# Kernel optimization log

Measured on AMD Instinct MI355X. Metric: run time of the kernel, lower is better.

## Reference

```python
import jax, jax.numpy as jnp
import numpy as np

B, T, V = 4096, 32, 256          # batch, decode steps, vocab
E, CE, H, L, NH = 768, 64, 256, 2, 4  # eword_dim, char_emb_dim, hidden, gru layers, heads
HD = H // NH                      # head dim
BOS, PAD = 1, 0


def _gru_cell(x, h, w_ih, w_hh, b_ih, b_hh):
    # PyTorch GRUCell math: gates ordered (r, z, n)
    gi = x @ w_ih.T + b_ih
    gh = h @ w_hh.T + b_hh
    ir, iz, inn = jnp.split(gi, 3, axis=-1)
    hr, hz, hn = jnp.split(gh, 3, axis=-1)
    r = jax.nn.sigmoid(ir + hr)
    z = jax.nn.sigmoid(iz + hz)
    n = jnp.tanh(inn + r * hn)
    return (1.0 - z) * n + z * h


def setup_inputs() -> dict:
    key = jax.random.key(0)
    ks = jax.random.split(key, 24)
    s = 0.02
    p = lambda k, shp: (jax.random.normal(k, shp, jnp.float32) * s)
    return {
        "eword": jax.random.normal(ks[0], (B, E), jnp.float32),
        "target_ids": jax.random.randint(ks[1], (B, T), 0, V),
        # params
        "char_emb": p(ks[2], (V, CE)).at[PAD].set(0.0),
        "eword_proj_w": p(ks[3], (H, E)), "eword_proj_b": p(ks[4], (H,)),
        "gru_w_ih0": p(ks[5], (3 * H, CE + E)), "gru_w_hh0": p(ks[6], (3 * H, H)),
        "gru_b_ih0": p(ks[7], (3 * H,)), "gru_b_hh0": p(ks[8], (3 * H,)),
        "gru_w_ih1": p(ks[9], (3 * H, H)), "gru_w_hh1": p(ks[10], (3 * H, H)),
        "gru_b_ih1": p(ks[11], (3 * H,)), "gru_b_hh1": p(ks[12], (3 * H,)),
        "attn_in_w": p(ks[13], (3 * H, H)), "attn_in_b": p(ks[14], (3 * H,)),
        "attn_out_w": p(ks[15], (H, H)), "attn_out_b": p(ks[16], (H,)),
        "key_w": p(ks[17], (H, E)), "key_b": p(ks[18], (H,)),
        "val_w": p(ks[19], (H, E)), "val_b": p(ks[20], (H,)),
        "proj_w": p(ks[21], (V, H)), "proj_b": p(ks[22], (V,)),
    }


def reference(eword, target_ids, char_emb, eword_proj_w, eword_proj_b,
              gru_w_ih0, gru_w_hh0, gru_b_ih0, gru_b_hh0,
              gru_w_ih1, gru_w_hh1, gru_b_ih1, gru_b_hh1,
              attn_in_w, attn_in_b, attn_out_w, attn_out_b,
              key_w, key_b, val_w, val_b, proj_w, proj_b):
    batch = eword.shape[0]
    # init hidden: tanh(Linear(eword)) broadcast across layers
    h0 = jnp.tanh(eword @ eword_proj_w.T + eword_proj_b)
    # pre-projected key/value (seq len 1), then MHA in-proj for k,v (static)
    wq, wk, wv = jnp.split(attn_in_w, 3, axis=0)
    bq, bk, bv = jnp.split(attn_in_b, 3)
    ek = (eword @ key_w.T + key_b) @ wk.T + bk        # (B, H)
    ev = (eword @ val_w.T + val_b) @ wv.T + bv        # (B, H)
    kh = ek.reshape(batch, NH, HD)                     # (B, NH, HD)
    vh = ev.reshape(batch, NH, HD)
    scale = 1.0 / np.sqrt(HD).astype(np.float32)

    # teacher forcing: input at step t is BOS for t=0, else target_ids[:, t-1]
    in_ids = jnp.concatenate(
        [jnp.full((batch, 1), BOS, target_ids.dtype), target_ids[:, :-1]], axis=1)

    def step(carry, ids):
        h_l0, h_l1 = carry
        ce = char_emb[ids] * (ids != PAD)[:, None].astype(char_emb.dtype)
        x = jnp.concatenate([ce, eword], axis=-1)     # (B, CE+E)
        h_l0 = _gru_cell(x, h_l0, gru_w_ih0, gru_w_hh0, gru_b_ih0, gru_b_hh0)
        h_l1 = _gru_cell(h_l0, h_l1, gru_w_ih1, gru_w_hh1, gru_b_ih1, gru_b_hh1)
        # single-query cross-attention over a length-1 key/value
        q = (h_l1 @ wq.T + bq).reshape(batch, NH, HD)
        score = jnp.sum(q * kh, axis=-1, keepdims=True) * scale  # (B, NH, 1)
        w = jax.nn.softmax(score, axis=-1)            # ones (len-1 softmax)
        attn = (w * vh).reshape(batch, H)
        attn_out = attn @ attn_out_w.T + attn_out_b
        out = h_l1 + attn_out
        logits = out @ proj_w.T + proj_b              # (B, V)
        return (h_l0, h_l1), logits

    _, logits_t = jax.lax.scan(step, (h0, h0), in_ids.T)  # (T, B, V)
    return jnp.transpose(logits_t, (1, 0, 2))              # (B, T, V)
```

## Files before the change

kernel.cpp:

```cpp
#include <hip/hip_runtime.h>


typedef __bf16 bf16;
typedef __attribute__((ext_vector_type(8))) __bf16 bf16x8;
typedef __attribute__((ext_vector_type(4))) __bf16 bf16x4;
typedef __attribute__((ext_vector_type(4))) float fx4;

#define MFMA16(a, b, c) __builtin_amdgcn_mfma_f32_16x16x32_bf16(a, b, c, 0, 0, 0)

__device__ __forceinline__ float sigm(float x) { return 1.0f / (1.0f + expf(-x)); }

__device__ __forceinline__ bf16x8 cvt8(const float* __restrict__ p) {
    float4 u = ((const float4*)p)[0];
    float4 v = ((const float4*)p)[1];
    bf16x8 r;
    r[0] = (bf16)u.x; r[1] = (bf16)u.y; r[2] = (bf16)u.z; r[3] = (bf16)u.w;
    r[4] = (bf16)v.x; r[5] = (bf16)v.y; r[6] = (bf16)v.z; r[7] = (bf16)v.w;
    return r;
}

__device__ __forceinline__ bf16x8 addcvt8(bf16x8 h, const float* __restrict__ p) {
    float4 u = ((const float4*)p)[0];
    float4 v = ((const float4*)p)[1];
    bf16x8 r;
    r[0] = (bf16)((float)h[0] + u.x); r[1] = (bf16)((float)h[1] + u.y);
    r[2] = (bf16)((float)h[2] + u.z); r[3] = (bf16)((float)h[3] + u.w);
    r[4] = (bf16)((float)h[4] + v.x); r[5] = (bf16)((float)h[5] + v.y);
    r[6] = (bf16)((float)h[6] + v.z); r[7] = (bf16)((float)h[7] + v.w);
    return r;
}

__global__ void f2b(const float* __restrict__ s, bf16* __restrict__ d, int n) {
    int i = (blockIdx.x * 256 + threadIdx.x) * 4;
    if (i >= n) return;
    float4 v = *(const float4*)(s + i);
    bf16x4 o;
    o[0] = (bf16)v.x; o[1] = (bf16)v.y; o[2] = (bf16)v.z; o[3] = (bf16)v.w;
    *(bf16x4*)(d + i) = o;
}

__global__ void wpack(const float* __restrict__ src, bf16* __restrict__ dst) {
    int gid = blockIdx.x * 256 + threadIdx.x;
    if (gid >= 768 * 32) return;
    int gc = gid >> 5, piece = gid & 31;
    int g = gc >> 8, rem = gc & 255, w = rem >> 4, l16 = rem & 15;
    int c = piece >> 2, quad = piece & 3;
    bf16x8 v = cvt8(src + (size_t)gc * 256 + piece * 8);
    size_t d = (size_t)w * 12288 + (size_t)(c * 3 + g) * 512 + l16 * 32 + quad * 8;
    *(bf16x8*)(dst + d) = v;
}

__global__ __launch_bounds__(256, 4) void gemm_bt(
    const float* __restrict__ A, int lda,
    const float* __restrict__ W, int ldw,
    const float* __restrict__ bias,
    float* __restrict__ out, int ldo, int act_tanh, int K)
{
    const int tid  = threadIdx.x;
    const int wid  = tid >> 6;
    const int lane = tid & 63;
    const int quad = lane >> 4;
    const int l16  = lane & 15;
    const int m0   = blockIdx.x * 32;
    const int n0   = blockIdx.y * 256 + wid * 64;

    fx4 acc[4][2];
#pragma unroll
    for (int j = 0; j < 4; ++j) {
        acc[j][0] = fx4{0.f, 0.f, 0.f, 0.f};
        acc[j][1] = fx4{0.f, 0.f, 0.f, 0.f};
    }

    const float* a0p = A + (size_t)(m0 + l16) * lda + quad * 8;
    const float* a1p = A + (size_t)(m0 + 16 + l16) * lda + quad * 8;

    for (int k0 = 0; k0 < K; k0 += 32) {
        bf16x8 a0 = cvt8(a0p + k0);
        bf16x8 a1 = cvt8(a1p + k0);
#pragma unroll
        for (int j = 0; j < 4; ++j) {
            bf16x8 b = cvt8(W + (size_t)(n0 + j * 16 + l16) * ldw + k0 + quad * 8);
            acc[j][0] = MFMA16(a0, b, acc[j][0]);
            acc[j][1] = MFMA16(a1, b, acc[j][1]);
        }
    }

#pragma unroll
    for (int j = 0; j < 4; ++j) {
        int n = n0 + j * 16 + l16;
        float bv = bias ? bias[n] : 0.0f;
#pragma unroll
        for (int rt = 0; rt < 2; ++rt)
#pragma unroll
            for (int r = 0; r < 4; ++r) {
                int m = m0 + rt * 16 + quad * 4 + r;
                float v = acc[j][rt][r] + bv;
                if (act_tanh) v = tanhf(v);
                out[(size_t)m * ldo + n] = v;
            }
    }
}

__global__ __launch_bounds__(1024, 4) void decoder_loop(
    const int*   __restrict__ tgt,
    const float* __restrict__ h0i,
    const float* __restrict__ gword,
    const float* __restrict__ cproj,
    const bf16*  __restrict__ w_hh0p, const float* __restrict__ b_hh0,
    const bf16*  __restrict__ w_ih1p, const float* __restrict__ b_ih1,
    const bf16*  __restrict__ w_hh1p, const float* __restrict__ b_hh1,
    bf16* __restrict__ h1all)
{
    __shared__ __align__(16) bf16 hb0[2][16][264];
    __shared__ __align__(16) bf16 hb1[2][16][264];

    const int tid  = threadIdx.x;
    const int wid  = tid >> 6;
    const int lane = tid & 63;
    const int quad = lane >> 4;
    const int l16  = lane & 15;
    const int row0 = blockIdx.x * 16;
    const int col  = wid * 16 + l16;
    const int rw   = quad * 4;

    const bf16* pW0 = w_hh0p + (size_t)wid * 12288 + l16 * 32 + quad * 8;
    const bf16* pW1 = w_ih1p + (size_t)wid * 12288 + l16 * 32 + quad * 8;
    const bf16* pW2 = w_hh1p + (size_t)wid * 12288 + l16 * 32 + quad * 8;

    float h0m[4], h1m[4], cg[3][4];
    float bh0[3], bi1[3], bh1[3];
#pragma unroll
    for (int g = 0; g < 3; ++g) {
        bh0[g] = b_hh0[g * 256 + col];
        bi1[g] = b_ih1[g * 256 + col];
        bh1[g] = b_hh1[g * 256 + col];
    }
#pragma unroll
    for (int r = 0; r < 4; ++r) {
        int row = row0 + rw + r;
        float v = h0i[(size_t)row * 256 + col];
        h0m[r] = v; h1m[r] = v;
        bf16 bv = (bf16)v;
        hb0[0][rw + r][col] = bv; hb1[0][rw + r][col] = bv;
#pragma unroll
        for (int g = 0; g < 3; ++g)
            cg[g][r] = cproj[(size_t)768 + g * 256 + col]
                     + gword[(size_t)row * 768 + g * 256 + col];
    }

    __syncthreads();

    for (int t = 0; t < 32; ++t) {
        const int p = t & 1, q = p ^ 1;

        fx4 g0[3], g1[3];
#pragma unroll
        for (int g = 0; g < 3; ++g) {
            g0[g] = fx4{0.f, 0.f, 0.f, 0.f};
            g1[g] = fx4{0.f, 0.f, 0.f, 0.f};
        }
        bf16x8 a_c, c_c, w0[3], w2[3];
        a_c = *(const bf16x8*)&hb0[p][l16][quad * 8];
        c_c = *(const bf16x8*)&hb1[p][l16][quad * 8];
#pragma unroll
        for (int g = 0; g < 3; ++g) {
            w0[g] = *(const bf16x8*)(pW0 + g * 512);
            w2[g] = *(const bf16x8*)(pW2 + g * 512);
        }
#pragma unroll
        for (int kk = 0; kk < 8; ++kk) {
            bf16x8 a_n, c_n, w0n[3], w2n[3];
            if (kk < 7) {
                a_n = *(const bf16x8*)&hb0[p][l16][(kk + 1) * 32 + quad * 8];
                c_n = *(const bf16x8*)&hb1[p][l16][(kk + 1) * 32 + quad * 8];
#pragma unroll
                for (int g = 0; g < 3; ++g) {
                    w0n[g] = *(const bf16x8*)(pW0 + ((kk + 1) * 3 + g) * 512);
                    w2n[g] = *(const bf16x8*)(pW2 + ((kk + 1) * 3 + g) * 512);
                }
            }
#pragma unroll
            for (int g = 0; g < 3; ++g) {
                g0[g] = MFMA16(a_c, w0[g], g0[g]);
                g1[g] = MFMA16(c_c, w2[g], g1[g]);
            }
            if (kk < 7) {
                a_c = a_n; c_c = c_n;
#pragma unroll
                for (int g = 0; g < 3; ++g) { w0[g] = w0n[g]; w2[g] = w2n[g]; }
            }
        }
#pragma unroll
        for (int r = 0; r < 4; ++r) {
            float rr = sigm(cg[0][r] + g0[0][r] + bh0[0]);
            float zz = sigm(cg[1][r] + g0[1][r] + bh0[1]);
            float nn = tanhf(cg[2][r] + rr * (g0[2][r] + bh0[2]));
            h0m[r] = (1.0f - zz) * nn + zz * h0m[r];
            hb0[q][rw + r][col] = (bf16)h0m[r];
        }
        __syncthreads();

        int nid[4];
#pragma unroll
        for (int r = 0; r < 4; ++r)
            nid[r] = tgt[(row0 + rw + r) * 32 + t];
        float cgn[3][4];
#pragma unroll
        for (int g = 0; g < 3; ++g)
#pragma unroll
            for (int r = 0; r < 4; ++r)
                cgn[g][r] = cproj[(size_t)nid[r] * 768 + g * 256 + col]
                          + gword[(size_t)(row0 + rw + r) * 768 + g * 256 + col];

        fx4 gi[3];
#pragma unroll
        for (int g = 0; g < 3; ++g) gi[g] = fx4{0.f, 0.f, 0.f, 0.f};
        bf16x8 b_c, w1[3];
        b_c = *(const bf16x8*)&hb0[q][l16][quad * 8];
#pragma unroll
        for (int g = 0; g < 3; ++g)
            w1[g] = *(const bf16x8*)(pW1 + g * 512);
#pragma unroll
        for (int kk = 0; kk < 8; ++kk) {
            bf16x8 b_n, w1n[3];
            if (kk < 7) {
                b_n = *(const bf16x8*)&hb0[q][l16][(kk + 1) * 32 + quad * 8];
#pragma unroll
                for (int g = 0; g < 3; ++g)
                    w1n[g] = *(const bf16x8*)(pW1 + ((kk + 1) * 3 + g) * 512);
            }
#pragma unroll
            for (int g = 0; g < 3; ++g)
                gi[g] = MFMA16(b_c, w1[g], gi[g]);
            if (kk < 7) {
                b_c = b_n;
#pragma unroll
                for (int g = 0; g < 3; ++g) w1[g] = w1n[g];
            }
        }
#pragma unroll
        for (int r = 0; r < 4; ++r) {
            float rr = sigm(gi[0][r] + bi1[0] + g1[0][r] + bh1[0]);
            float zz = sigm(gi[1][r] + bi1[1] + g1[1][r] + bh1[1]);
            float nn = tanhf(gi[2][r] + bi1[2] + rr * (g1[2][r] + bh1[2]));
            h1m[r] = (1.0f - zz) * nn + zz * h1m[r];
            bf16 hv = (bf16)h1m[r];
            hb1[q][rw + r][col] = hv;
            __builtin_nontemporal_store(
                hv, &h1all[((size_t)(row0 + rw + r) * 32 + t) * 256 + col]);
        }
#pragma unroll
        for (int g = 0; g < 3; ++g)
#pragma unroll
            for (int r = 0; r < 4; ++r) cg[g][r] = cgn[g][r];

        __syncthreads();
    }
}

__global__ __launch_bounds__(256, 4) void logits_final(
    const bf16*  __restrict__ h1,
    const float* __restrict__ a2,
    const bf16*  __restrict__ pw,
    const float* __restrict__ pb,
    float* __restrict__ out)
{
    const int tid  = threadIdx.x;
    const int wid  = tid >> 6;
    const int lane = tid & 63;
    const int quad = lane >> 4;
    const int l16  = lane & 15;
    const int m0   = blockIdx.x * 32;
    const int n0   = wid * 64;
    const int b    = m0 >> 5;

    fx4 acc[4][2];
#pragma unroll
    for (int j = 0; j < 4; ++j) {
        acc[j][0] = fx4{0.f, 0.f, 0.f, 0.f};
        acc[j][1] = fx4{0.f, 0.f, 0.f, 0.f};
    }

    for (int k0 = 0; k0 < 256; k0 += 32) {
        bf16x8 h0 = *(const bf16x8*)(h1 + (size_t)(m0 + l16) * 256 + k0 + quad * 8);
        bf16x8 h1v = *(const bf16x8*)(h1 + (size_t)(m0 + 16 + l16) * 256 + k0 + quad * 8);
        const float* ap = a2 + (size_t)b * 256 + k0 + quad * 8;
        bf16x8 a0 = addcvt8(h0, ap);
        bf16x8 a1 = addcvt8(h1v, ap);
#pragma unroll
        for (int j = 0; j < 4; ++j) {
            bf16x8 bb = *(const bf16x8*)(pw + (size_t)(n0 + j * 16 + l16) * 256 + k0 + quad * 8);
            acc[j][0] = MFMA16(a0, bb, acc[j][0]);
            acc[j][1] = MFMA16(a1, bb, acc[j][1]);
        }
    }

#pragma unroll
    for (int j = 0; j < 4; ++j) {
        int n = n0 + j * 16 + l16;
        float bv = pb[n];
#pragma unroll
        for (int rt = 0; rt < 2; ++rt)
#pragma unroll
            for (int r = 0; r < 4; ++r) {
                int m = m0 + rt * 16 + quad * 4 + r;
                out[(size_t)m * 256 + n] = acc[j][rt][r] + bv;
            }
    }
}

extern "C" void kernel_launch(void* const* d_in, const int* in_sizes, int n_in,
                              void* d_out, int out_size, void* d_ws, size_t ws_size,
                              hipStream_t stream)
{
    const float* eword      = (const float*)d_in[0];
    const int*   tgt        = (const int*)  d_in[1];
    const float* char_emb   = (const float*)d_in[2];
    const float* ew_w       = (const float*)d_in[3];
    const float* ew_b       = (const float*)d_in[4];
    const float* w_ih0      = (const float*)d_in[5];
    const float* w_hh0      = (const float*)d_in[6];
    const float* b_ih0      = (const float*)d_in[7];
    const float* b_hh0      = (const float*)d_in[8];
    const float* w_ih1      = (const float*)d_in[9];
    const float* w_hh1      = (const float*)d_in[10];
    const float* b_ih1      = (const float*)d_in[11];
    const float* b_hh1      = (const float*)d_in[12];
    const float* attn_in_w  = (const float*)d_in[13];
    const float* attn_in_b  = (const float*)d_in[14];
    const float* attn_out_w = (const float*)d_in[15];
    const float* attn_out_b = (const float*)d_in[16];
    const float* val_w      = (const float*)d_in[19];
    const float* val_b      = (const float*)d_in[20];
    const float* proj_w     = (const float*)d_in[21];
    const float* proj_b     = (const float*)d_in[22];

    char* ws = (char*)d_ws;
    float* h0i   = (float*)ws;  ws += (size_t)4096 * 256 * 4;
    float* gwrd  = (float*)ws;  ws += (size_t)4096 * 768 * 4;
    float* cproj = (float*)ws;  ws += (size_t)256  * 768 * 4;
    float* a2    = (float*)ws;  ws += (size_t)4096 * 256 * 4;
    float* buf1  = (float*)ws;  ws += (size_t)4096 * 256 * 4;
    float* buf2  = (float*)ws;  ws += (size_t)4096 * 256 * 4;
    bf16*  wbhh0 = (bf16*)ws;   ws += (size_t)768 * 256 * 2;
    bf16*  wbih1 = (bf16*)ws;   ws += (size_t)768 * 256 * 2;
    bf16*  wbhh1 = (bf16*)ws;   ws += (size_t)768 * 256 * 2;
    bf16*  wbprj = (bf16*)ws;   ws += (size_t)256 * 256 * 2;
    bf16*  h1all = (bf16*)ws;   ws += (size_t)4096 * 32 * 256 * 2;

    dim3 blk(256);
    wpack<<<dim3(96), blk, 0, stream>>>(w_hh0, wbhh0);
    wpack<<<dim3(96), blk, 0, stream>>>(w_ih1, wbih1);
    wpack<<<dim3(96), blk, 0, stream>>>(w_hh1, wbhh1);
    f2b<<<dim3(64),  blk, 0, stream>>>(proj_w, wbprj, 256 * 256);

    gemm_bt<<<dim3(128, 1), blk, 0, stream>>>(eword, 768, ew_w, 768, ew_b, h0i, 256, 1, 768);
    gemm_bt<<<dim3(128, 3), blk, 0, stream>>>(eword, 768, w_ih0 + 64, 832, b_ih0, gwrd, 768, 0, 768);
    gemm_bt<<<dim3(8, 3),   blk, 0, stream>>>(char_emb, 64, w_ih0, 832, nullptr, cproj, 768, 0, 64);
    gemm_bt<<<dim3(128, 1), blk, 0, stream>>>(eword, 768, val_w, 768, val_b, buf1, 256, 0, 768);
    gemm_bt<<<dim3(128, 1), blk, 0, stream>>>(buf1, 256, attn_in_w + 512 * 256, 256, attn_in_b + 512, buf2, 256, 0, 256);
    gemm_bt<<<dim3(128, 1), blk, 0, stream>>>(buf2, 256, attn_out_w, 256, attn_out_b, a2, 256, 0, 256);

    decoder_loop<<<dim3(256), dim3(1024), 0, stream>>>(
        tgt, h0i, gwrd, cproj,
        wbhh0, b_hh0, wbih1, b_ih1, wbhh1, b_hh1, h1all);

    logits_final<<<dim3(4096), blk, 0, stream>>>(h1all, a2, wbprj, proj_b, (float*)d_out);
}
```

Measured before the change: 2.236 ms.

## Process 32 rows per decoder block and stage gate inputs in bf16

Each decoder block now handles 32 batch rows instead of 16, so every recurrent weight fragment loaded from memory feeds two MFMAs, and the grid shrinks to 128 blocks. The precomputed eword and char-embedding gate projections are converted to bf16 by extra kernels before the loop, halving their per-step gather traffic. The hidden state is now kept only as bf16 in shared memory instead of fp32 registers. This removes the software prefetch of weights, leaves half as many blocks as there are compute units, and adds bf16 rounding to the recurrent state and gate inputs.

```diff
diff --git a/kernel.cpp b/kernel.cpp
--- a/kernel.cpp
+++ b/kernel.cpp
@@ -104,30 +104,28 @@
 __global__ __launch_bounds__(1024, 4) void decoder_loop(
     const int*   __restrict__ tgt,
     const float* __restrict__ h0i,
-    const float* __restrict__ gword,
-    const float* __restrict__ cproj,
+    const bf16*  __restrict__ gwb,
+    const bf16*  __restrict__ cpb,
     const bf16*  __restrict__ w_hh0p, const float* __restrict__ b_hh0,
     const bf16*  __restrict__ w_ih1p, const float* __restrict__ b_ih1,
     const bf16*  __restrict__ w_hh1p, const float* __restrict__ b_hh1,
     bf16* __restrict__ h1all)
 {
-    __shared__ __align__(16) bf16 hb0[2][16][264];
-    __shared__ __align__(16) bf16 hb1[2][16][264];
+    __shared__ __align__(16) bf16 hb0[2][32][264];
+    __shared__ __align__(16) bf16 hb1[2][32][264];
 
     const int tid  = threadIdx.x;
     const int wid  = tid >> 6;
     const int lane = tid & 63;
     const int quad = lane >> 4;
     const int l16  = lane & 15;
-    const int row0 = blockIdx.x * 16;
+    const int row0 = blockIdx.x * 32;
     const int col  = wid * 16 + l16;
-    const int rw   = quad * 4;
 
     const bf16* pW0 = w_hh0p + (size_t)wid * 12288 + l16 * 32 + quad * 8;
     const bf16* pW1 = w_ih1p + (size_t)wid * 12288 + l16 * 32 + quad * 8;
     const bf16* pW2 = w_hh1p + (size_t)wid * 12288 + l16 * 32 + quad * 8;
 
-    float h0m[4], h1m[4], cg[3][4];
     float bh0[3], bi1[3], bh1[3];
 #pragma unroll
     for (int g = 0; g < 3; ++g) {
@@ -135,125 +133,100 @@
         bi1[g] = b_ih1[g * 256 + col];
         bh1[g] = b_hh1[g * 256 + col];
     }
-#pragma unroll
-    for (int r = 0; r < 4; ++r) {
-        int row = row0 + rw + r;
-        float v = h0i[(size_t)row * 256 + col];
-        h0m[r] = v; h1m[r] = v;
+
+#pragma unroll
+    for (int i = 0; i < 8; ++i) {
+        int row_l = (i >> 2) * 16 + quad * 4 + (i & 3);
+        float v = h0i[(size_t)(row0 + row_l) * 256 + col];
         bf16 bv = (bf16)v;
-        hb0[0][rw + r][col] = bv; hb1[0][rw + r][col] = bv;
-#pragma unroll
-        for (int g = 0; g < 3; ++g)
-            cg[g][r] = cproj[(size_t)768 + g * 256 + col]
-                     + gword[(size_t)row * 768 + g * 256 + col];
-    }
-
+        hb0[0][row_l][col] = bv;
+        hb1[0][row_l][col] = bv;
+    }
     __syncthreads();
 
     for (int t = 0; t < 32; ++t) {
         const int p = t & 1, q = p ^ 1;
 
-        fx4 g0[3], g1[3];
+        int ids[8];
+#pragma unroll
+        for (int i = 0; i < 8; ++i) {
+            int row_l = (i >> 2) * 16 + quad * 4 + (i & 3);
+            ids[i] = (t == 0) ? 1 : tgt[(row0 + row_l) * 32 + (t - 1)];
+        }
+        float cgv[3][8];
+#pragma unroll
+        for (int i = 0; i < 8; ++i) {
+            int row_l = (i >> 2) * 16 + quad * 4 + (i & 3);
+#pragma unroll
+            for (int g = 0; g < 3; ++g)
+                cgv[g][i] = (float)cpb[(size_t)ids[i] * 768 + g * 256 + col]
+                          + (float)gwb[(size_t)(row0 + row_l) * 768 + g * 256 + col];
+        }
+
+        fx4 g0[3][2];
 #pragma unroll
         for (int g = 0; g < 3; ++g) {
-            g0[g] = fx4{0.f, 0.f, 0.f, 0.f};
-            g1[g] = fx4{0.f, 0.f, 0.f, 0.f};
-        }
-        bf16x8 a_c, c_c, w0[3], w2[3];
-        a_c = *(const bf16x8*)&hb0[p][l16][quad * 8];
-        c_c = *(const bf16x8*)&hb1[p][l16][quad * 8];
+            g0[g][0] = fx4{0.f, 0.f, 0.f, 0.f};
+            g0[g][1] = fx4{0.f, 0.f, 0.f, 0.f};
+        }
+#pragma unroll
+        for (int kk = 0; kk < 8; ++kk) {
+            bf16x8 a0 = *(const bf16x8*)&hb0[p][l16][kk * 32 + quad * 8];
+            bf16x8 a1 = *(const bf16x8*)&hb0[p][16 + l16][kk * 32 + quad * 8];
+#pragma unroll
+            for (int g = 0; g < 3; ++g) {
+                bf16x8 w = *(const bf16x8*)(pW0 + (kk * 3 + g) * 512);
+                g0[g][0] = MFMA16(a0, w, g0[g][0]);
+                g0[g][1] = MFMA16(a1, w, g0[g][1]);
+            }
+        }
+#pragma unroll
+        for (int i = 0; i < 8; ++i) {
+            int rt = i >> 2, r = i & 3;
+            int row_l = rt * 16 + quad * 4 + r;
+            float hold = (float)hb0[p][row_l][col];
+            float rr = sigm(cgv[0][i] + g0[0][rt][r] + bh0[0]);
+            float zz = sigm(cgv[1][i] + g0[1][rt][r] + bh0[1]);
+            float nn = tanhf(cgv[2][i] + rr * (g0[2][rt][r] + bh0[2]));
+            hb0[q][row_l][col] = (bf16)((1.0f - zz) * nn + zz * hold);
+        }
+        __syncthreads();
+
+        fx4 gi[3][2], gh[3][2];
 #pragma unroll
         for (int g = 0; g < 3; ++g) {
-            w0[g] = *(const bf16x8*)(pW0 + g * 512);
-            w2[g] = *(const bf16x8*)(pW2 + g * 512);
+            gi[g][0] = fx4{0.f, 0.f, 0.f, 0.f}; gi[g][1] = fx4{0.f, 0.f, 0.f, 0.f};
+            gh[g][0] = fx4{0.f, 0.f, 0.f, 0.f}; gh[g][1] = fx4{0.f, 0.f, 0.f, 0.f};
         }
 #pragma unroll
         for (int kk = 0; kk < 8; ++kk) {
-            bf16x8 a_n, c_n, w0n[3], w2n[3];
-            if (kk < 7) {
-                a_n = *(const bf16x8*)&hb0[p][l16][(kk + 1) * 32 + quad * 8];
-                c_n = *(const bf16x8*)&hb1[p][l16][(kk + 1) * 32 + quad * 8];
-#pragma unroll
-                for (int g = 0; g < 3; ++g) {
-                    w0n[g] = *(const bf16x8*)(pW0 + ((kk + 1) * 3 + g) * 512);
-                    w2n[g] = *(const bf16x8*)(pW2 + ((kk + 1) * 3 + g) * 512);
-                }
+            bf16x8 a0 = *(const bf16x8*)&hb0[q][l16][kk * 32 + quad * 8];
+            bf16x8 a1 = *(const bf16x8*)&hb0[q][16 + l16][kk * 32 + quad * 8];
+            bf16x8 c0 = *(const bf16x8*)&hb1[p][l16][kk * 32 + quad * 8];
+            bf16x8 c1 = *(const bf16x8*)&hb1[p][16 + l16][kk * 32 + quad * 8];
+#pragma unroll
+            for (int g = 0; g < 3; ++g) {
+                bf16x8 w1 = *(const bf16x8*)(pW1 + (kk * 3 + g) * 512);
+                gi[g][0] = MFMA16(a0, w1, gi[g][0]);
+                gi[g][1] = MFMA16(a1, w1, gi[g][1]);
+                bf16x8 w2 = *(const bf16x8*)(pW2 + (kk * 3 + g) * 512);
+                gh[g][0] = MFMA16(c0, w2, gh[g][0]);
+                gh[g][1] = MFMA16(c1, w2, gh[g][1]);
             }
-#pragma unroll
-            for (int g = 0; g < 3; ++g) {
-                g0[g] = MFMA16(a_c, w0[g], g0[g]);
-                g1[g] = MFMA16(c_c, w2[g], g1[g]);
-            }
-            if (kk < 7) {
-                a_c = a_n; c_c = c_n;
-#pragma unroll
-                for (int g = 0; g < 3; ++g) { w0[g] = w0n[g]; w2[g] = w2n[g]; }
-            }
-        }
-#pragma unroll
-        for (int r = 0; r < 4; ++r) {
-            float rr = sigm(cg[0][r] + g0[0][r] + bh0[0]);
-            float zz = sigm(cg[1][r] + g0[1][r] + bh0[1]);
-            float nn = tanhf(cg[2][r] + rr * (g0[2][r] + bh0[2]));
-            h0m[r] = (1.0f - zz) * nn + zz * h0m[r];
-            hb0[q][rw + r][col] = (bf16)h0m[r];
-        }
-        __syncthreads();
-
-        int nid[4];
-#pragma unroll
-        for (int r = 0; r < 4; ++r)
-            nid[r] = tgt[(row0 + rw + r) * 32 + t];
-        float cgn[3][4];
-#pragma unroll
-        for (int g = 0; g < 3; ++g)
-#pragma unroll
-            for (int r = 0; r < 4; ++r)
-                cgn[g][r] = cproj[(size_t)nid[r] * 768 + g * 256 + col]
-                          + gword[(size_t)(row0 + rw + r) * 768 + g * 256 + col];
-
-        fx4 gi[3];
-#pragma unroll
-        for (int g = 0; g < 3; ++g) gi[g] = fx4{0.f, 0.f, 0.f, 0.f};
-        bf16x8 b_c, w1[3];
-        b_c = *(const bf16x8*)&hb0[q][l16][quad * 8];
-#pragma unroll
-        for (int g = 0; g < 3; ++g)
-            w1[g] = *(const bf16x8*)(pW1 + g * 512);
-#pragma unroll
-        for (int kk = 0; kk < 8; ++kk) {
-            bf16x8 b_n, w1n[3];
-            if (kk < 7) {
-                b_n = *(const bf16x8*)&hb0[q][l16][(kk + 1) * 32 + quad * 8];
-#pragma unroll
-                for (int g = 0; g < 3; ++g)
-                    w1n[g] = *(const bf16x8*)(pW1 + ((kk + 1) * 3 + g) * 512);
-            }
-#pragma unroll
-            for (int g = 0; g < 3; ++g)
-                gi[g] = MFMA16(b_c, w1[g], gi[g]);
-            if (kk < 7) {
-                b_c = b_n;
-#pragma unroll
-                for (int g = 0; g < 3; ++g) w1[g] = w1n[g];
-            }
-        }
-#pragma unroll
-        for (int r = 0; r < 4; ++r) {
-            float rr = sigm(gi[0][r] + bi1[0] + g1[0][r] + bh1[0]);
-            float zz = sigm(gi[1][r] + bi1[1] + g1[1][r] + bh1[1]);
-            float nn = tanhf(gi[2][r] + bi1[2] + rr * (g1[2][r] + bh1[2]));
-            h1m[r] = (1.0f - zz) * nn + zz * h1m[r];
-            bf16 hv = (bf16)h1m[r];
-            hb1[q][rw + r][col] = hv;
+        }
+#pragma unroll
+        for (int i = 0; i < 8; ++i) {
+            int rt = i >> 2, r = i & 3;
+            int row_l = rt * 16 + quad * 4 + r;
+            float hold = (float)hb1[p][row_l][col];
+            float rr = sigm(gi[0][rt][r] + bi1[0] + gh[0][rt][r] + bh1[0]);
+            float zz = sigm(gi[1][rt][r] + bi1[1] + gh[1][rt][r] + bh1[1]);
+            float nn = tanhf(gi[2][rt][r] + bi1[2] + rr * (gh[2][rt][r] + bh1[2]));
+            bf16 hv = (bf16)((1.0f - zz) * nn + zz * hold);
+            hb1[q][row_l][col] = hv;
             __builtin_nontemporal_store(
-                hv, &h1all[((size_t)(row0 + rw + r) * 32 + t) * 256 + col]);
-        }
-#pragma unroll
-        for (int g = 0; g < 3; ++g)
-#pragma unroll
-            for (int r = 0; r < 4; ++r) cg[g][r] = cgn[g][r];
-
+                hv, &h1all[((size_t)(row0 + row_l) * 32 + t) * 256 + col]);
+        }
         __syncthreads();
     }
 }
@@ -340,8 +313,11 @@
     float* gwrd  = (float*)ws;  ws += (size_t)4096 * 768 * 4;
     float* cproj = (float*)ws;  ws += (size_t)256  * 768 * 4;
     float* a2    = (float*)ws;  ws += (size_t)4096 * 256 * 4;
-    float* buf1  = (float*)ws;  ws += (size_t)4096 * 256 * 4;
-    float* buf2  = (float*)ws;  ws += (size_t)4096 * 256 * 4;
+    char*  hreg  = ws;          ws += (size_t)8 * 1024 * 1024;
+    float* buf1  = (float*)hreg;
+    float* buf2  = (float*)(hreg + (size_t)4*1024*1024);
+    bf16*  gwb   = (bf16*)hreg;
+    bf16*  cpb   = (bf16*)(hreg + (size_t)6*1024*1024);
     bf16*  wbhh0 = (bf16*)ws;   ws += (size_t)768 * 256 * 2;
     bf16*  wbih1 = (bf16*)ws;   ws += (size_t)768 * 256 * 2;
     bf16*  wbhh1 = (bf16*)ws;   ws += (size_t)768 * 256 * 2;
@@ -361,8 +337,11 @@
     gemm_bt<<<dim3(128, 1), blk, 0, stream>>>(buf1, 256, attn_in_w + 512 * 256, 256, attn_in_b + 512, buf2, 256, 0, 256);
     gemm_bt<<<dim3(128, 1), blk, 0, stream>>>(buf2, 256, attn_out_w, 256, attn_out_b, a2, 256, 0, 256);
 
-    decoder_loop<<<dim3(256), dim3(1024), 0, stream>>>(
-        tgt, h0i, gwrd, cproj,
+    f2b<<<dim3(3072), blk, 0, stream>>>(gwrd, gwb, 4096 * 768);
+    f2b<<<dim3(192),  blk, 0, stream>>>(cproj, cpb, 256 * 768);
+
+    decoder_loop<<<dim3(128), dim3(1024), 0, stream>>>(
+        tgt, h0i, gwb, cpb,
         wbhh0, b_hh0, wbih1, b_ih1, wbhh1, b_hh1, h1all);
 
     logits_final<<<dim3(4096), blk, 0, stream>>>(h1all, a2, wbprj, proj_b, (float*)d_out);
```

Result: slower. 2.373 ms (+6.1%).

## Shrink decoder blocks to 4 waves with packed bf16 gate inputs and fast activations

Applied to the files above, without the earlier changes.

The recurrent decoder now runs 256-thread blocks in which each wave computes 64 hidden columns (four column groups) instead of 16-wave blocks with one group per wave. Per-step input gates (eword projection plus char projection) are prepacked into interleaved bf16x4 tables with the biases folded in. The tables are read each step rather than kept in fp32 registers, and the old hidden state is read back from LDS instead of kept in registers. Sigmoid and tanh use __expf and a hardware reciprocal. This trades parallelism per block (fewer waves per CU, longer serial MFMA chains per wave) for fewer synchronisation participants and less register state, and adds bf16 rounding of the gate inputs and the carried hidden state.

```diff
diff --git a/kernel.cpp b/kernel.cpp
--- a/kernel.cpp
+++ b/kernel.cpp
@@ -8,7 +8,9 @@
 
 #define MFMA16(a, b, c) __builtin_amdgcn_mfma_f32_16x16x32_bf16(a, b, c, 0, 0, 0)
 
-__device__ __forceinline__ float sigm(float x) { return 1.0f / (1.0f + expf(-x)); }
+__device__ __forceinline__ float fastrcp(float x) { return __builtin_amdgcn_rcpf(x); }
+__device__ __forceinline__ float sigm_f(float x) { return fastrcp(1.0f + __expf(-x)); }
+__device__ __forceinline__ float tanh_f(float x) { return 1.0f - 2.0f * fastrcp(__expf(2.0f * x) + 1.0f); }
 
 __device__ __forceinline__ bf16x8 cvt8(const float* __restrict__ p) {
     float4 u = ((const float4*)p)[0];
@@ -48,6 +50,39 @@
     bf16x8 v = cvt8(src + (size_t)gc * 256 + piece * 8);
     size_t d = (size_t)w * 12288 + (size_t)(c * 3 + g) * 512 + l16 * 32 + quad * 8;
     *(bf16x8*)(dst + d) = v;
+}
+
+__global__ void gpack(const float* __restrict__ g, const float* __restrict__ bhh0,
+                      bf16* __restrict__ o) {
+    int i = blockIdx.x * 256 + threadIdx.x;
+    if (i >= 4096 * 256) return;
+    int row = i >> 8, col = i & 255;
+    const float* s = g + (size_t)row * 768 + col;
+    bf16x4 v;
+    v[0] = (bf16)(s[0]   + bhh0[col]);
+    v[1] = (bf16)(s[256] + bhh0[256 + col]);
+    v[2] = (bf16)(s[512]);
+    v[3] = (bf16)0.0f;
+    *(bf16x4*)(o + (size_t)i * 4) = v;
+}
+
+__global__ void cpack(const float* __restrict__ c, bf16* __restrict__ o) {
+    int i = blockIdx.x * 256 + threadIdx.x;
+    if (i >= 256 * 256) return;
+    int row = i >> 8, col = i & 255;
+    const float* s = c + (size_t)row * 768 + col;
+    bf16x4 v;
+    v[0] = (bf16)s[0]; v[1] = (bf16)s[256]; v[2] = (bf16)s[512]; v[3] = (bf16)0.0f;
+    *(bf16x4*)(o + (size_t)i * 4) = v;
+}
+
+__global__ void bprep(const float* __restrict__ bi1, const float* __restrict__ bh1,
+                      const float* __restrict__ bhh0,
+                      float4* __restrict__ biasT, float* __restrict__ bh0n) {
+    int c = threadIdx.x;
+    biasT[c] = make_float4(bi1[c] + bh1[c], bi1[256 + c] + bh1[256 + c],
+                           bi1[512 + c], bh1[512 + c]);
+    bh0n[c] = bhh0[512 + c];
 }
 
 __global__ __launch_bounds__(256, 4) void gemm_bt(
@@ -101,159 +136,149 @@
     }
 }
 
-__global__ __launch_bounds__(1024, 4) void decoder_loop(
+__global__ __launch_bounds__(256, 1) void decoder_loop(
     const int*   __restrict__ tgt,
     const float* __restrict__ h0i,
-    const float* __restrict__ gword,
-    const float* __restrict__ cproj,
-    const bf16*  __restrict__ w_hh0p, const float* __restrict__ b_hh0,
-    const bf16*  __restrict__ w_ih1p, const float* __restrict__ b_ih1,
-    const bf16*  __restrict__ w_hh1p, const float* __restrict__ b_hh1,
+    const bf16*  __restrict__ gwb2,
+    const bf16*  __restrict__ cpb2,
+    const bf16*  __restrict__ w_hh0p,
+    const bf16*  __restrict__ w_ih1p,
+    const bf16*  __restrict__ w_hh1p,
+    const float4* __restrict__ biasT,
+    const float* __restrict__ bh0nT,
     bf16* __restrict__ h1all)
 {
     __shared__ __align__(16) bf16 hb0[2][16][264];
     __shared__ __align__(16) bf16 hb1[2][16][264];
 
     const int tid  = threadIdx.x;
-    const int wid  = tid >> 6;
+    const int w    = tid >> 6;
     const int lane = tid & 63;
     const int quad = lane >> 4;
     const int l16  = lane & 15;
     const int row0 = blockIdx.x * 16;
-    const int col  = wid * 16 + l16;
     const int rw   = quad * 4;
 
-    const bf16* pW0 = w_hh0p + (size_t)wid * 12288 + l16 * 32 + quad * 8;
-    const bf16* pW1 = w_ih1p + (size_t)wid * 12288 + l16 * 32 + quad * 8;
-    const bf16* pW2 = w_hh1p + (size_t)wid * 12288 + l16 * 32 + quad * 8;
-
-    float h0m[4], h1m[4], cg[3][4];
-    float bh0[3], bi1[3], bh1[3];
-#pragma unroll
-    for (int g = 0; g < 3; ++g) {
-        bh0[g] = b_hh0[g * 256 + col];
-        bi1[g] = b_ih1[g * 256 + col];
-        bh1[g] = b_hh1[g * 256 + col];
-    }
-#pragma unroll
-    for (int r = 0; r < 4; ++r) {
-        int row = row0 + rw + r;
-        float v = h0i[(size_t)row * 256 + col];
-        h0m[r] = v; h1m[r] = v;
-        bf16 bv = (bf16)v;
-        hb0[0][rw + r][col] = bv; hb1[0][rw + r][col] = bv;
-#pragma unroll
-        for (int g = 0; g < 3; ++g)
-            cg[g][r] = cproj[(size_t)768 + g * 256 + col]
-                     + gword[(size_t)row * 768 + g * 256 + col];
-    }
-
+    const int lofs = l16 * 32 + quad * 8;
+    const bf16* pW0 = w_hh0p + (size_t)(4 * w) * 12288 + lofs;
+    const bf16* pW1 = w_ih1p + (size_t)(4 * w) * 12288 + lofs;
+    const bf16* pW2 = w_hh1p + (size_t)(4 * w) * 12288 + lofs;
+
+    float4 bT[4]; float b0n[4];
+#pragma unroll
+    for (int cg = 0; cg < 4; ++cg) {
+        int colw = w * 64 + cg * 16 + l16;
+        bT[cg]  = biasT[colw];
+        b0n[cg] = bh0nT[colw];
+    }
+
+#pragma unroll
+    for (int cg = 0; cg < 4; ++cg)
+#pragma unroll
+        for (int r = 0; r < 4; ++r) {
+            int colw = w * 64 + cg * 16 + l16;
+            float v = h0i[(size_t)(row0 + rw + r) * 256 + colw];
+            bf16 b = (bf16)v;
+            hb0[0][rw + r][colw] = b;
+            hb1[0][rw + r][colw] = b;
+        }
     __syncthreads();
 
     for (int t = 0; t < 32; ++t) {
         const int p = t & 1, q = p ^ 1;
 
-        fx4 g0[3], g1[3];
-#pragma unroll
-        for (int g = 0; g < 3; ++g) {
-            g0[g] = fx4{0.f, 0.f, 0.f, 0.f};
-            g1[g] = fx4{0.f, 0.f, 0.f, 0.f};
-        }
-        bf16x8 a_c, c_c, w0[3], w2[3];
-        a_c = *(const bf16x8*)&hb0[p][l16][quad * 8];
-        c_c = *(const bf16x8*)&hb1[p][l16][quad * 8];
-#pragma unroll
-        for (int g = 0; g < 3; ++g) {
-            w0[g] = *(const bf16x8*)(pW0 + g * 512);
-            w2[g] = *(const bf16x8*)(pW2 + g * 512);
-        }
+        int ids[4];
+#pragma unroll
+        for (int r = 0; r < 4; ++r)
+            ids[r] = (t == 0) ? 1 : tgt[(row0 + rw + r) * 32 + (t - 1)];
+        float cgr[4][4], cgz[4][4], cgn[4][4];
+#pragma unroll
+        for (int cg = 0; cg < 4; ++cg)
+#pragma unroll
+            for (int r = 0; r < 4; ++r) {
+                int colw = w * 64 + cg * 16 + l16;
+                bf16x4 gv = *(const bf16x4*)(gwb2 + ((size_t)(row0 + rw + r) * 256 + colw) * 4);
+                bf16x4 cv = *(const bf16x4*)(cpb2 + ((size_t)ids[r] * 256 + colw) * 4);
+                cgr[cg][r] = (float)gv[0] + (float)cv[0];
+                cgz[cg][r] = (float)gv[1] + (float)cv[1];
+                cgn[cg][r] = (float)gv[2] + (float)cv[2];
+            }
+
+        fx4 g0[4][3];
+#pragma unroll
+        for (int cg = 0; cg < 4; ++cg)
+#pragma unroll
+            for (int g = 0; g < 3; ++g) g0[cg][g] = fx4{0.f, 0.f, 0.f, 0.f};
 #pragma unroll
         for (int kk = 0; kk < 8; ++kk) {
-            bf16x8 a_n, c_n, w0n[3], w2n[3];
-            if (kk < 7) {
-                a_n = *(const bf16x8*)&hb0[p][l16][(kk + 1) * 32 + quad * 8];
-                c_n = *(const bf16x8*)&hb1[p][l16][(kk + 1) * 32 + quad * 8];
+            bf16x8 a = *(const bf16x8*)&hb0[p][l16][kk * 32 + quad * 8];
+#pragma unroll
+            for (int cg = 0; cg < 4; ++cg)
 #pragma unroll
                 for (int g = 0; g < 3; ++g) {
-                    w0n[g] = *(const bf16x8*)(pW0 + ((kk + 1) * 3 + g) * 512);
-                    w2n[g] = *(const bf16x8*)(pW2 + ((kk + 1) * 3 + g) * 512);
+                    bf16x8 wv = *(const bf16x8*)(pW0 + cg * 12288 + (kk * 3 + g) * 512);
+                    g0[cg][g] = MFMA16(a, wv, g0[cg][g]);
                 }
-            }
+        }
+#pragma unroll
+        for (int cg = 0; cg < 4; ++cg) {
+            int colw = w * 64 + cg * 16 + l16;
+#pragma unroll
+            for (int r = 0; r < 4; ++r) {
+                float hold = (float)hb0[p][rw + r][colw];
+                float rr = sigm_f(cgr[cg][r] + g0[cg][0][r]);
+                float zz = sigm_f(cgz[cg][r] + g0[cg][1][r]);
+                float nn = tanh_f(cgn[cg][r] + rr * (g0[cg][2][r] + b0n[cg]));
+                hb0[q][rw + r][colw] = (bf16)((1.0f - zz) * nn + zz * hold);
+            }
+        }
+        __syncthreads();
+
+        fx4 gi[4][3], gh[4][3];
+#pragma unroll
+        for (int cg = 0; cg < 4; ++cg)
 #pragma unroll
             for (int g = 0; g < 3; ++g) {
-                g0[g] = MFMA16(a_c, w0[g], g0[g]);
-                g1[g] = MFMA16(c_c, w2[g], g1[g]);
-            }
-            if (kk < 7) {
-                a_c = a_n; c_c = c_n;
-#pragma unroll
-                for (int g = 0; g < 3; ++g) { w0[g] = w0n[g]; w2[g] = w2n[g]; }
-            }
-        }
-#pragma unroll
-        for (int r = 0; r < 4; ++r) {
-            float rr = sigm(cg[0][r] + g0[0][r] + bh0[0]);
-            float zz = sigm(cg[1][r] + g0[1][r] + bh0[1]);
-            float nn = tanhf(cg[2][r] + rr * (g0[2][r] + bh0[2]));
-            h0m[r] = (1.0f - zz) * nn + zz * h0m[r];
-            hb0[q][rw + r][col] = (bf16)h0m[r];
-        }
-        __syncthreads();
-
-        int nid[4];
-#pragma unroll
-        for (int r = 0; r < 4; ++r)
-            nid[r] = tgt[(row0 + rw + r) * 32 + t];
-        float cgn[3][4];
-#pragma unroll
-        for (int g = 0; g < 3; ++g)
-#pragma unroll
-            for (int r = 0; r < 4; ++r)
-                cgn[g][r] = cproj[(size_t)nid[r] * 768 + g * 256 + col]
-                          + gword[(size_t)(row0 + rw + r) * 768 + g * 256 + col];
-
-        fx4 gi[3];
-#pragma unroll
-        for (int g = 0; g < 3; ++g) gi[g] = fx4{0.f, 0.f, 0.f, 0.f};
-        bf16x8 b_c, w1[3];
-        b_c = *(const bf16x8*)&hb0[q][l16][quad * 8];
-#pragma unroll
-        for (int g = 0; g < 3; ++g)
-            w1[g] = *(const bf16x8*)(pW1 + g * 512);
+                gi[cg][g] = fx4{0.f, 0.f, 0.f, 0.f};
+                gh[cg][g] = fx4{0.f, 0.f, 0.f, 0.f};
+            }
 #pragma unroll
         for (int kk = 0; kk < 8; ++kk) {
-            bf16x8 b_n, w1n[3];
-            if (kk < 7) {
-                b_n = *(const bf16x8*)&hb0[q][l16][(kk + 1) * 32 + quad * 8];
-#pragma unroll
-                for (int g = 0; g < 3; ++g)
-                    w1n[g] = *(const bf16x8*)(pW1 + ((kk + 1) * 3 + g) * 512);
-            }
-#pragma unroll
-            for (int g = 0; g < 3; ++g)
-                gi[g] = MFMA16(b_c, w1[g], gi[g]);
-            if (kk < 7) {
-                b_c = b_n;
-#pragma unroll
-                for (int g = 0; g < 3; ++g) w1[g] = w1n[g];
-            }
-        }
-#pragma unroll
-        for (int r = 0; r < 4; ++r) {
-            float rr = sigm(gi[0][r] + bi1[0] + g1[0][r] + bh1[0]);
-            float zz = sigm(gi[1][r] + bi1[1] + g1[1][r] + bh1[1]);
-            float nn = tanhf(gi[2][r] + bi1[2] + rr * (g1[2][r] + bh1[2]));
-            h1m[r] = (1.0f - zz) * nn + zz * h1m[r];
-            bf16 hv = (bf16)h1m[r];
-            hb1[q][rw + r][col] = hv;
-            __builtin_nontemporal_store(
-                hv, &h1all[((size_t)(row0 + rw + r) * 32 + t) * 256 + col]);
-        }
-#pragma unroll
-        for (int g = 0; g < 3; ++g)
-#pragma unroll
-            for (int r = 0; r < 4; ++r) cg[g][r] = cgn[g][r];
-
+            bf16x8 a = *(const bf16x8*)&hb0[q][l16][kk * 32 + quad * 8];
+#pragma unroll
+            for (int cg = 0; cg < 4; ++cg)
+#pragma unroll
+                for (int g = 0; g < 3; ++g) {
+                    bf16x8 wv = *(const bf16x8*)(pW1 + cg * 12288 + (kk * 3 + g) * 512);
+                    gi[cg][g] = MFMA16(a, wv, gi[cg][g]);
+                }
+        }
+#pragma unroll
+        for (int kk = 0; kk < 8; ++kk) {
+            bf16x8 c = *(const bf16x8*)&hb1[p][l16][kk * 32 + quad * 8];
+#pragma unroll
+            for (int cg = 0; cg < 4; ++cg)
+#pragma unroll
+                for (int g = 0; g < 3; ++g) {
+                    bf16x8 wv = *(const bf16x8*)(pW2 + cg * 12288 + (kk * 3 + g) * 512);
+                    gh[cg][g] = MFMA16(c, wv, gh[cg][g]);
+                }
+        }
+#pragma unroll
+        for (int cg = 0; cg < 4; ++cg) {
+            int colw = w * 64 + cg * 16 + l16;
+#pragma unroll
+            for (int r = 0; r < 4; ++r) {
+                float hold = (float)hb1[p][rw + r][colw];
+                float rr = sigm_f(gi[cg][0][r] + gh[cg][0][r] + bT[cg].x);
+                float zz = sigm_f(gi[cg][1][r] + gh[cg][1][r] + bT[cg].y);
+                float nn = tanh_f(gi[cg][2][r] + bT[cg].z + rr * (gh[cg][2][r] + bT[cg].w));
+                bf16 hv = (bf16)((1.0f - zz) * nn + zz * hold);
+                hb1[q][rw + r][colw] = hv;
+                __builtin_nontemporal_store(
+                    hv, &h1all[((size_t)(row0 + rw + r) * 32 + t) * 256 + colw]);
+            }
+        }
         __syncthreads();
     }
 }
@@ -340,12 +365,17 @@
     float* gwrd  = (float*)ws;  ws += (size_t)4096 * 768 * 4;
     float* cproj = (float*)ws;  ws += (size_t)256  * 768 * 4;
     float* a2    = (float*)ws;  ws += (size_t)4096 * 256 * 4;
-    float* buf1  = (float*)ws;  ws += (size_t)4096 * 256 * 4;
-    float* buf2  = (float*)ws;  ws += (size_t)4096 * 256 * 4;
+    char*  hreg  = ws;          ws += (size_t)8 * 1024 * 1024;
+    float* buf1  = (float*)hreg;
+    float* buf2  = (float*)(hreg + (size_t)4*1024*1024);
+    bf16*  gwb2  = (bf16*)hreg;
+    bf16*  cpb2  = (bf16*)ws;   ws += (size_t)256 * 256 * 4 * 2;
     bf16*  wbhh0 = (bf16*)ws;   ws += (size_t)768 * 256 * 2;
     bf16*  wbih1 = (bf16*)ws;   ws += (size_t)768 * 256 * 2;
     bf16*  wbhh1 = (bf16*)ws;   ws += (size_t)768 * 256 * 2;
     bf16*  wbprj = (bf16*)ws;   ws += (size_t)256 * 256 * 2;
+    float4* biasT = (float4*)ws; ws += 256 * 16;
+    float* bh0nT = (float*)ws;  ws += 256 * 4;
     bf16*  h1all = (bf16*)ws;   ws += (size_t)4096 * 32 * 256 * 2;
 
     dim3 blk(256);
@@ -353,6 +383,7 @@
     wpack<<<dim3(96), blk, 0, stream>>>(w_ih1, wbih1);
     wpack<<<dim3(96), blk, 0, stream>>>(w_hh1, wbhh1);
     f2b<<<dim3(64),  blk, 0, stream>>>(proj_w, wbprj, 256 * 256);
+    bprep<<<dim3(1), blk, 0, stream>>>(b_ih1, b_hh1, b_hh0, biasT, bh0nT);
 
     gemm_bt<<<dim3(128, 1), blk, 0, stream>>>(eword, 768, ew_w, 768, ew_b, h0i, 256, 1, 768);
     gemm_bt<<<dim3(128, 3), blk, 0, stream>>>(eword, 768, w_ih0 + 64, 832, b_ih0, gwrd, 768, 0, 768);
@@ -361,9 +392,11 @@
     gemm_bt<<<dim3(128, 1), blk, 0, stream>>>(buf1, 256, attn_in_w + 512 * 256, 256, attn_in_b + 512, buf2, 256, 0, 256);
     gemm_bt<<<dim3(128, 1), blk, 0, stream>>>(buf2, 256, attn_out_w, 256, attn_out_b, a2, 256, 0, 256);
 
-    decoder_loop<<<dim3(256), dim3(1024), 0, stream>>>(
-        tgt, h0i, gwrd, cproj,
-        wbhh0, b_hh0, wbih1, b_ih1, wbhh1, b_hh1, h1all);
+    gpack<<<dim3(4096), blk, 0, stream>>>(gwrd, b_hh0, gwb2);
+    cpack<<<dim3(256),  blk, 0, stream>>>(cproj, cpb2);
+
+    decoder_loop<<<dim3(256), blk, 0, stream>>>(
+        tgt, h0i, gwb2, cpb2, wbhh0, wbih1, wbhh1, biasT, bh0nT, h1all);
 
     logits_final<<<dim3(4096), blk, 0, stream>>>(h1all, a2, wbprj, proj_b, (float*)d_out);
 }
```

Result: slower. 3.693 ms (+65.1%).
